# Kernel tuning notes

Measured on AMD Instinct MI355X. Metric: run time of the kernel, lower is better.

Reference implementation:

```python
import jax, jax.numpy as jnp
import numpy as np

C = 256       # in_channels
IC = 128      # inter_channels = C // 2
G = 4         # num_group
D = IC // G   # per-group channels = 32
B, H, W_ = 4, 56, 56
EPS = 1e-5


def conv1x1(x, w, b=None):
    # x: (B,Cin,H,W), w: (Cout,Cin)
    y = jnp.einsum('bchw,oc->bohw', x, w)
    if b is not None:
        y = y + b[None, :, None, None]
    return y


def bn(x, scale, bias, mean, var):
    inv = scale / jnp.sqrt(var + EPS)
    return x * inv[None, :, None, None] + (bias - mean * inv)[None, :, None, None]


def setup_inputs():
    key = jax.random.key(0)
    ks = jax.random.split(key, 16)
    r = lambda k, shape, s=0.05: jax.random.normal(k, shape, jnp.float32) * s
    C4 = C // 4
    return {
        'x': jax.random.normal(ks[0], (B, C, H, W_), jnp.float32),
        'g_w': r(ks[1], (IC, C)), 'g_b': r(ks[2], (IC,)),
        'theta_w': r(ks[3], (IC, C)), 'theta_b': r(ks[4], (IC,)),
        'phi_w': r(ks[5], (IC, C)), 'phi_b': r(ks[6], (IC,)),
        'W_w': r(ks[7], (C, IC)), 'W_b': r(ks[8], (C,)),
        'bnW_scale': jnp.ones((C,)), 'bnW_bias': jnp.zeros((C,)),
        'bnW_mean': jnp.zeros((C,)), 'bnW_var': jnp.ones((C,)),
        'ff1_w': r(ks[9], (C4, C)),
        'ffbn1_scale': jnp.ones((C4,)), 'ffbn1_bias': jnp.zeros((C4,)),
        'ffbn1_mean': jnp.zeros((C4,)), 'ffbn1_var': jnp.ones((C4,)),
        'ff2_w': r(ks[10], (C4, C4, 3, 3)),
        'ffbn2_scale': jnp.ones((C4,)), 'ffbn2_bias': jnp.zeros((C4,)),
        'ffbn2_mean': jnp.zeros((C4,)), 'ffbn2_var': jnp.ones((C4,)),
        'ff3_w': r(ks[11], (C, C4)),
        'ffbn3_scale': jnp.ones((C,)), 'ffbn3_bias': jnp.zeros((C,)),
        'ffbn3_mean': jnp.zeros((C,)), 'ffbn3_var': jnp.ones((C,)),
    }


def reference(x, g_w, g_b, theta_w, theta_b, phi_w, phi_b, W_w, W_b,
              bnW_scale, bnW_bias, bnW_mean, bnW_var,
              ff1_w, ffbn1_scale, ffbn1_bias, ffbn1_mean, ffbn1_var,
              ff2_w, ffbn2_scale, ffbn2_bias, ffbn2_mean, ffbn2_var,
              ff3_w, ffbn3_scale, ffbn3_bias, ffbn3_mean, ffbn3_var):
    b, c, h, w = x.shape
    n = h * w
    # grouped non-local attention: channels split into G groups of D
    gx = conv1x1(x, g_w, g_b).reshape(b, G, D, n)       # (B,G,D,N)
    tx = conv1x1(x, theta_w, theta_b).reshape(b, G, D, n)
    px = conv1x1(x, phi_w, phi_b).reshape(b, G, D, n)
    f = jnp.einsum('bgdn,bgdm->bgnm', tx, px)           # (B,G,N,N) scores
    attn = jax.nn.softmax(f, axis=-1)                   # softmax over keys (torch dim=2 on (b,N,N))
    yy = jnp.einsum('bgnm,bgdm->bgdn', attn, gx)        # (B,G,D,N)
    y_out = yy.reshape(b, IC, h, w)
    W_y = bn(conv1x1(y_out, W_w, W_b), bnW_scale, bnW_bias, bnW_mean, bnW_var)
    z = jax.nn.relu(W_y + x)
    # FPNFFConv bottleneck FFN (BN in eval mode)
    o = jax.nn.relu(bn(conv1x1(z, ff1_w), ffbn1_scale, ffbn1_bias, ffbn1_mean, ffbn1_var))
    o = jax.lax.conv_general_dilated(o, ff2_w, (1, 1), 'SAME',
                                     dimension_numbers=('NCHW', 'OIHW', 'NCHW'))
    o = jax.nn.relu(bn(o, ffbn2_scale, ffbn2_bias, ffbn2_mean, ffbn2_var))
    o = bn(conv1x1(o, ff3_w), ffbn3_scale, ffbn3_bias, ffbn3_mean, ffbn3_var)
    return jax.nn.relu(o + z)
```

## Files before the change

### kernel.cpp

```cpp
#include <hip/hip_runtime.h>
#include <hip/hip_bf16.h>

#define NPIX 3136
#define BB 4
#define LOG2E 1.4426950408889634f

typedef unsigned short u16;
typedef __bf16 bf16x8 __attribute__((ext_vector_type(8)));
typedef float f32x4 __attribute__((ext_vector_type(4)));

__device__ __forceinline__ float b2f(u16 u) {
  union { unsigned u; float f; } c; c.u = ((unsigned)u) << 16; return c.f;
}
__device__ __forceinline__ u16 f2b(float f) {
  __hip_bfloat16 h = __float2bfloat16(f);
  return *reinterpret_cast<u16*>(&h);
}
__device__ __forceinline__ unsigned pk2(float a, float b) {
  return (unsigned)f2b(a) | ((unsigned)f2b(b) << 16);
}
__device__ __forceinline__ f32x4 mfma(bf16x8 a, bf16x8 b, f32x4 c) {
  return __builtin_amdgcn_mfma_f32_16x16x32_bf16(a, b, c, 0, 0, 0);
}

template<int NSTEP, int NOT>
__device__ __forceinline__ void mf_gemm2(const u16* __restrict__ A0,
                                         const u16* __restrict__ A1,
                                         const u16* __restrict__ Brow, int sB,
                                         int lq, f32x4* acc) {
#pragma unroll
  for (int s = 0; s < NSTEP; ++s) {
    bf16x8 bf[NOT];
#pragma unroll
    for (int ot = 0; ot < NOT; ++ot)
      bf[ot] = *(const bf16x8*)(Brow + (size_t)ot * 16 * sB + s * 32 + lq * 8);
    bf16x8 a0 = *(const bf16x8*)(A0 + s * 32 + lq * 8);
    bf16x8 a1 = *(const bf16x8*)(A1 + s * 32 + lq * 8);
#pragma unroll
    for (int ot = 0; ot < NOT; ++ot) {
      acc[ot] = mfma(a0, bf[ot], acc[ot]);
      acc[NOT + ot] = mfma(a1, bf[ot], acc[NOT + ot]);
    }
  }
}

__global__ __launch_bounds__(256) void prep_kernel(
    const float* __restrict__ x, u16* __restrict__ xt,
    const float* __restrict__ gw, const float* __restrict__ tw,
    const float* __restrict__ pw, const float* __restrict__ Ww,
    const float* __restrict__ f1w, const float* __restrict__ f2w,
    const float* __restrict__ f3w,
    u16* __restrict__ gwb, u16* __restrict__ twb, u16* __restrict__ pwb,
    u16* __restrict__ Wwb, u16* __restrict__ f1b, u16* __restrict__ f3b,
    u16* __restrict__ f2p) {
  __shared__ u16 sT[64 * 65];
  const int id = blockIdx.x;
  if (id < 784) {
    const int b = id / 196, rest = id % 196;
    const int c0 = (rest / 49) * 64, n0 = (rest % 49) * 64;
    const int t = threadIdx.x;
#pragma unroll
    for (int cc = 0; cc < 4; ++cc) {
      int c = cc * 16 + (t >> 4), n4 = (t & 15) * 4;
      float4 v = *(const float4*)(x + ((size_t)(b * 256 + c0 + c)) * NPIX + n0 + n4);
      sT[c * 65 + n4 + 0] = f2b(v.x);
      sT[c * 65 + n4 + 1] = f2b(v.y);
      sT[c * 65 + n4 + 2] = f2b(v.z);
      sT[c * 65 + n4 + 3] = f2b(v.w);
    }
    __syncthreads();
#pragma unroll
    for (int nn = 0; nn < 4; ++nn) {
      int n = nn * 16 + (t >> 4), c4 = (t & 15) * 4;
      uint2 s;
      s.x = (unsigned)sT[(c4 + 0) * 65 + n] | ((unsigned)sT[(c4 + 1) * 65 + n] << 16);
      s.y = (unsigned)sT[(c4 + 2) * 65 + n] | ((unsigned)sT[(c4 + 3) * 65 + n] << 16);
      *(uint2*)(xt + ((size_t)b * NPIX + n0 + n) * 256 + c0 + c4) = s;
    }
  } else {
    for (int i = (id - 784) * 256 + threadIdx.x; i < 200704; i += 196 * 256) {
      int j = i;
      if (j < 32768) { gwb[j] = f2b(gw[j]); continue; } j -= 32768;
      if (j < 32768) { twb[j] = f2b(tw[j] * LOG2E); continue; } j -= 32768;
      if (j < 32768) { pwb[j] = f2b(pw[j]); continue; } j -= 32768;
      if (j < 32768) { Wwb[j] = f2b(Ww[j]); continue; } j -= 32768;
      if (j < 16384) { f1b[j] = f2b(f1w[j]); continue; } j -= 16384;
      if (j < 16384) { f3b[j] = f2b(f3w[j]); continue; } j -= 16384;
      int t = j >> 12, rem = j & 4095, co = rem >> 6, ci = rem & 63;
      f2p[j] = f2b(f2w[(co * 64 + ci) * 9 + t]);
    }
  }
}

__global__ __launch_bounds__(256) void proj_kernel(
    const u16* __restrict__ xt,
    const u16* __restrict__ gwb, const u16* __restrict__ twb, const u16* __restrict__ pwb,
    const float* __restrict__ gb, const float* __restrict__ tb, const float* __restrict__ pb,
    u16* __restrict__ gx, u16* __restrict__ Tq, u16* __restrict__ Pk) {
  const int b = blockIdx.z, oc = blockIdx.y, nb = blockIdx.x * 128;
  const int sec = oc >> 1, rbase = (oc & 1) * 64;
  const u16* wsel = sec == 0 ? gwb : (sec == 1 ? twb : pwb);
  const float* bsel = sec == 0 ? gb : (sec == 1 ? tb : pb);
  const int wv = threadIdx.x >> 6, lane = threadIdx.x & 63;
  const int lr = lane & 15, lq = lane >> 4;
  const int nrow0 = nb + wv * 32, nrow1 = nrow0 + 16;
  const int r0 = nrow0 + lr < NPIX ? nrow0 + lr : NPIX - 1;
  const int r1 = nrow1 + lr < NPIX ? nrow1 + lr : NPIX - 1;
  f32x4 acc[8] = {};
  mf_gemm2<8, 4>(xt + ((size_t)b * NPIX + r0) * 256,
                 xt + ((size_t)b * NPIX + r1) * 256,
                 wsel + (size_t)(rbase + lr) * 256, 256, lq, acc);
#pragma unroll
  for (int t = 0; t < 2; ++t) {
    const int qn = (t ? nrow1 : nrow0) + lq * 4;
    if (qn >= NPIX) continue;
#pragma unroll
    for (int ot = 0; ot < 4; ++ot) {
      const f32x4 a = acc[t * 4 + ot];
      const int o = rbase + ot * 16 + lr;
      float bias = bsel[o];
      if (sec == 1) bias *= LOG2E;
      if (sec == 0) {
        uint2 s;
        s.x = pk2(a[0] + bias, a[1] + bias);
        s.y = pk2(a[2] + bias, a[3] + bias);
        *(uint2*)(gx + ((size_t)b * 128 + o) * NPIX + qn) = s;
      } else {
        const int g = o >> 5, dl = o & 31;
        u16* dst = sec == 1 ? Tq : Pk;
        size_t base = (size_t)(b * 4 + g) * NPIX;
#pragma unroll
        for (int r = 0; r < 4; ++r)
          dst[(base + qn + r) * 32 + dl] = f2b(a[r] + bias);
      }
    }
  }
}

__global__ __launch_bounds__(256) void attn_kernel(
    const u16* __restrict__ Tq, const u16* __restrict__ Pk,
    const u16* __restrict__ gx, u16* __restrict__ OPb, float* __restrict__ LP) {
  __shared__ __align__(16) u16 Plds[4][32][40];
  const int bid = blockIdx.x;
  const int ks = bid / 400, rem = bid % 400;
  const int bg = rem / 25, qblk = rem % 25;
  const int b = bg >> 2, g = bg & 3;
  const int wave = threadIdx.x >> 6, lane = threadIdx.x & 63;
  const int lr = lane & 15, lq = lane >> 4;
  const int qbase = qblk * 128 + wave * 32;
  const int kc0 = ks * 448;
  const u16* Qp = Tq + (size_t)bg * NPIX * 32;
  const u16* Kp = Pk + (size_t)bg * NPIX * 32;
  const u16* Vp = gx + ((size_t)b * 128 + g * 32) * NPIX;

  bf16x8 qf[2];
#pragma unroll
  for (int qi = 0; qi < 2; ++qi) {
    int row = qbase + qi * 16 + lr;
    row = row < NPIX ? row : NPIX - 1;
    qf[qi] = *(const bf16x8*)(Qp + (size_t)row * 32 + lq * 8);
  }
  const f32x4 z4 = {0.f, 0.f, 0.f, 0.f};
  f32x4 O[2][2], Lf[2];
#pragma unroll
  for (int qi = 0; qi < 2; ++qi) { O[qi][0] = z4; O[qi][1] = z4; Lf[qi] = z4; }
  bf16x8 onef;
#pragma unroll
  for (int j = 0; j < 8; ++j) onef[j] = (__bf16)1.0f;

#pragma unroll 1
  for (int kc = kc0; kc < kc0 + 448; kc += 32) {
    bf16x8 kf0 = *(const bf16x8*)(Kp + (size_t)(kc + lr) * 32 + lq * 8);
    bf16x8 kf1 = *(const bf16x8*)(Kp + (size_t)(kc + 16 + lr) * 32 + lq * 8);
    f32x4 S[2][2];
    S[0][0] = mfma(qf[0], kf0, z4);
    S[0][1] = mfma(qf[0], kf1, z4);
    S[1][0] = mfma(qf[1], kf0, z4);
    S[1][1] = mfma(qf[1], kf1, z4);
#pragma unroll
    for (int qi = 0; qi < 2; ++qi)
#pragma unroll
      for (int kt = 0; kt < 2; ++kt)
#pragma unroll
        for (int r = 0; r < 4; ++r) {
          unsigned u = __builtin_bit_cast(unsigned, __builtin_exp2f(S[qi][kt][r]));
          Plds[wave][qi * 16 + lq * 4 + r][kt * 16 + lr] = (u16)(u >> 16);
        }
    bf16x8 pf0 = *(const bf16x8*)(&Plds[wave][lr][lq * 8]);
    bf16x8 pf1 = *(const bf16x8*)(&Plds[wave][16 + lr][lq * 8]);
    bf16x8 vf0 = *(const bf16x8*)(Vp + (size_t)lr * NPIX + kc + lq * 8);
    bf16x8 vf1 = *(const bf16x8*)(Vp + (size_t)(16 + lr) * NPIX + kc + lq * 8);
    O[0][0] = mfma(pf0, vf0, O[0][0]);
    O[0][1] = mfma(pf0, vf1, O[0][1]);
    O[1][0] = mfma(pf1, vf0, O[1][0]);
    O[1][1] = mfma(pf1, vf1, O[1][1]);
    Lf[0] = mfma(pf0, onef, Lf[0]);
    Lf[1] = mfma(pf1, onef, Lf[1]);
  }
  const size_t sbase = (size_t)(ks * 16 + bg) * NPIX;
#pragma unroll
  for (int qi = 0; qi < 2; ++qi) {
#pragma unroll
    for (int r = 0; r < 4; ++r) {
      int qrow = qbase + qi * 16 + lq * 4 + r;
      if (qrow < NPIX) {
        size_t ob = (sbase + qrow) * 32;
        OPb[ob + lr] = f2b(O[qi][0][r]);
        OPb[ob + 16 + lr] = f2b(O[qi][1][r]);
        if (lr == 0) LP[sbase + qrow] = Lf[qi][r];
      }
    }
  }
}

__global__ __launch_bounds__(512) void wz_kernel(
    const u16* __restrict__ OPb, const float* __restrict__ LP,
    const u16* __restrict__ Wwb, const float* __restrict__ Wb,
    const float* __restrict__ sc, const float* __restrict__ bi,
    const float* __restrict__ mu, const float* __restrict__ var,
    const float* __restrict__ x, u16* __restrict__ zt) {
  __shared__ float Ls[4][32];
  const int b = blockIdx.y, nb = blockIdx.x * 32;
  const int tid = threadIdx.x;
  if (tid < 128) {
    int g = tid >> 5, row = tid & 31;
    float l = 0.f;
#pragma unroll
    for (int ks = 0; ks < 7; ++ks)
      l += LP[(size_t)(ks * 16 + b * 4 + g) * NPIX + nb + row];
    Ls[g][row] = 1.0f / l;
  }
  __syncthreads();
  const int wave = tid >> 6, lane = tid & 63;
  const int lr = lane & 15, lq = lane >> 4;
  const int oc = wave & 3, tt = wave >> 2;
  const int nrow = nb + tt * 16;
  f32x4 acc[4][4] = {};
#pragma unroll
  for (int g = 0; g < 4; ++g) {
    bf16x8 bf[4];
#pragma unroll
    for (int ot = 0; ot < 4; ++ot)
      bf[ot] = *(const bf16x8*)(Wwb + (size_t)(oc * 64 + ot * 16 + lr) * 128 + g * 32 + lq * 8);
#pragma unroll
    for (int ks = 0; ks < 7; ++ks) {
      bf16x8 af = *(const bf16x8*)(OPb +
          ((size_t)(ks * 16 + b * 4 + g) * NPIX + nrow + lr) * 32 + lq * 8);
#pragma unroll
      for (int ot = 0; ot < 4; ++ot)
        acc[g][ot] = mfma(af, bf[ot], acc[g][ot]);
    }
  }
#pragma unroll
  for (int ot = 0; ot < 4; ++ot) {
    const int o = oc * 64 + ot * 16 + lr;
    float inv = sc[o] * rsqrtf(var[o] + 1e-5f);
    float off = bi[o] - mu[o] * inv + Wb[o] * inv;
    const int qn = nrow + lq * 4;
    float4 xr = *(const float4*)(x + ((size_t)b * 256 + o) * NPIX + qn);
    float xv[4] = {xr.x, xr.y, xr.z, xr.w};
#pragma unroll
    for (int r = 0; r < 4; ++r) {
      int row = tt * 16 + lq * 4 + r;
      float y = acc[0][ot][r] * Ls[0][row] + acc[1][ot][r] * Ls[1][row] +
                acc[2][ot][r] * Ls[2][row] + acc[3][ot][r] * Ls[3][row];
      float v = fmaxf(y * inv + off + xv[r], 0.f);
      zt[((size_t)b * NPIX + qn + r) * 256 + o] = f2b(v);
    }
  }
}

__global__ __launch_bounds__(256) void ff1_kernel(
    const u16* __restrict__ zt, const u16* __restrict__ f1b,
    const float* __restrict__ sc, const float* __restrict__ bi,
    const float* __restrict__ mu, const float* __restrict__ var,
    u16* __restrict__ o1t) {
  const int b = blockIdx.z, oc = blockIdx.y, nb = blockIdx.x * 128;
  const int wv = threadIdx.x >> 6, lane = threadIdx.x & 63;
  const int lr = lane & 15, lq = lane >> 4;
  const int nrow0 = nb + wv * 32, nrow1 = nrow0 + 16;
  const int r0 = nrow0 + lr < NPIX ? nrow0 + lr : NPIX - 1;
  const int r1 = nrow1 + lr < NPIX ? nrow1 + lr : NPIX - 1;
  f32x4 acc[4] = {};
  mf_gemm2<8, 2>(zt + ((size_t)b * NPIX + r0) * 256,
                 zt + ((size_t)b * NPIX + r1) * 256,
                 f1b + (size_t)(oc * 32 + lr) * 256, 256, lq, acc);
#pragma unroll
  for (int t = 0; t < 2; ++t) {
    const int qn = (t ? nrow1 : nrow0) + lq * 4;
    if (qn >= NPIX) continue;
#pragma unroll
    for (int ot = 0; ot < 2; ++ot) {
      const f32x4 a = acc[t * 2 + ot];
      const int o = oc * 32 + ot * 16 + lr;
      float inv = sc[o] * rsqrtf(var[o] + 1e-5f);
      float off = bi[o] - mu[o] * inv;
#pragma unroll
      for (int r = 0; r < 4; ++r) {
        float v = fmaxf(a[r] * inv + off, 0.f);
        o1t[((size_t)b * NPIX + qn + r) * 64 + o] = f2b(v);
      }
    }
  }
}

__global__ __launch_bounds__(256) void ff23_kernel(
    const u16* __restrict__ o1t, const u16* __restrict__ f2p,
    const float* __restrict__ s2, const float* __restrict__ bi2,
    const float* __restrict__ mu2, const float* __restrict__ var2,
    const u16* __restrict__ f3b,
    const float* __restrict__ s3, const float* __restrict__ bi3,
    const float* __restrict__ mu3, const float* __restrict__ var3,
    const u16* __restrict__ zt, float* __restrict__ out) {
  __shared__ __align__(16) u16 o2s[32][72];
  const int b = blockIdx.y, nb = blockIdx.x * 32;
  const int wv = threadIdx.x >> 6, lane = threadIdx.x & 63;
  const int lr = lane & 15, lq = lane >> 4;
  const int tt = wv >> 1, oh = wv & 1;
  const int n0 = nb + tt * 16 + lr;
  const int h0 = n0 / 56, w0 = n0 % 56;
  f32x4 acc2[2] = {};
#pragma unroll
  for (int t = 0; t < 9; ++t) {
    const int dh = t / 3 - 1, dw = t % 3 - 1;
    const bool valid = (h0 + dh) >= 0 && (h0 + dh) < 56 && (w0 + dw) >= 0 && (w0 + dw) < 56;
    const u16* A0 = o1t + ((size_t)b * NPIX + n0 + dh * 56 + dw) * 64;
    const u16* Br = f2p + (size_t)t * 4096 + (size_t)(oh * 32 + lr) * 64;
#pragma unroll
    for (int k2 = 0; k2 < 2; ++k2) {
      bf16x8 bf0 = *(const bf16x8*)(Br + k2 * 32 + lq * 8);
      bf16x8 bf1 = *(const bf16x8*)(Br + (size_t)16 * 64 + k2 * 32 + lq * 8);
      bf16x8 a0 = {};
      if (valid) a0 = *(const bf16x8*)(A0 + k2 * 32 + lq * 8);
      acc2[0] = mfma(a0, bf0, acc2[0]);
      acc2[1] = mfma(a0, bf1, acc2[1]);
    }
  }
#pragma unroll
  for (int ot = 0; ot < 2; ++ot) {
    const int o = oh * 32 + ot * 16 + lr;
    float inv = s2[o] * rsqrtf(var2[o] + 1e-5f);
    float off = bi2[o] - mu2[o] * inv;
#pragma unroll
    for (int r = 0; r < 4; ++r) {
      float v = fmaxf(acc2[ot][r] * inv + off, 0.f);
      o2s[tt * 16 + lq * 4 + r][o] = f2b(v);
    }
  }
  __syncthreads();
  const int obase = oh * 128;
  f32x4 acc3[8] = {};
#pragma unroll
  for (int s = 0; s < 2; ++s) {
    bf16x8 af = *(const bf16x8*)(&o2s[tt * 16 + lr][s * 32 + lq * 8]);
#pragma unroll
    for (int ot = 0; ot < 8; ++ot) {
      bf16x8 bf = *(const bf16x8*)(f3b + (size_t)(obase + ot * 16 + lr) * 64 + s * 32 + lq * 8);
      acc3[ot] = mfma(af, bf, acc3[ot]);
    }
  }
  const int qn = nb + tt * 16 + lq * 4;
#pragma unroll
  for (int ot = 0; ot < 8; ++ot) {
    const int o = obase + ot * 16 + lr;
    float inv = s3[o] * rsqrtf(var3[o] + 1e-5f);
    float off = bi3[o] - mu3[o] * inv;
    float4 s;
    float* sv = (float*)&s;
#pragma unroll
    for (int r = 0; r < 4; ++r) {
      float zres = b2f(zt[((size_t)b * NPIX + qn + r) * 256 + o]);
      sv[r] = fmaxf(acc3[ot][r] * inv + off + zres, 0.f);
    }
    *(float4*)(out + ((size_t)b * 256 + o) * NPIX + qn) = s;
  }
}

extern "C" void kernel_launch(void* const* d_in, const int* in_sizes, int n_in,
                              void* d_out, int out_size, void* d_ws, size_t ws_size,
                              hipStream_t stream) {
  const float* x    = (const float*)d_in[0];
  const float* gw   = (const float*)d_in[1];
  const float* gb   = (const float*)d_in[2];
  const float* tw   = (const float*)d_in[3];
  const float* tb   = (const float*)d_in[4];
  const float* pw   = (const float*)d_in[5];
  const float* pb   = (const float*)d_in[6];
  const float* Ww   = (const float*)d_in[7];
  const float* Wb   = (const float*)d_in[8];
  const float* bnWs = (const float*)d_in[9];
  const float* bnWb = (const float*)d_in[10];
  const float* bnWm = (const float*)d_in[11];
  const float* bnWv = (const float*)d_in[12];
  const float* f1w  = (const float*)d_in[13];
  const float* b1s  = (const float*)d_in[14];
  const float* b1b  = (const float*)d_in[15];
  const float* b1m  = (const float*)d_in[16];
  const float* b1v  = (const float*)d_in[17];
  const float* f2w  = (const float*)d_in[18];
  const float* b2s  = (const float*)d_in[19];
  const float* b2b  = (const float*)d_in[20];
  const float* b2m  = (const float*)d_in[21];
  const float* b2v  = (const float*)d_in[22];
  const float* f3w  = (const float*)d_in[23];
  const float* b3s  = (const float*)d_in[24];
  const float* b3b  = (const float*)d_in[25];
  const float* b3m  = (const float*)d_in[26];
  const float* b3v  = (const float*)d_in[27];
  float* out = (float*)d_out;

  u16* p = (u16*)d_ws;
  u16* xt  = p; p += (size_t)BB * NPIX * 256;
  u16* gwb = p; p += 128 * 256;
  u16* twb = p; p += 128 * 256;
  u16* pwb = p; p += 128 * 256;
  u16* Wwb = p; p += 256 * 128;
  u16* f1b = p; p += 64 * 256;
  u16* f3b = p; p += 256 * 64;
  u16* f2p = p; p += 9 * 64 * 64;
  u16* Tq  = p; p += (size_t)16 * NPIX * 32;
  u16* Pk  = p; p += (size_t)16 * NPIX * 32;
  u16* gx  = p; p += (size_t)BB * 128 * NPIX;
  u16* OPb = p; p += (size_t)7 * 16 * NPIX * 32;
  float* LP = (float*)p; p += (size_t)7 * 16 * NPIX * 2;
  u16* zt  = p; p += (size_t)BB * NPIX * 256;
  u16* o1t = p; p += (size_t)BB * NPIX * 64;

  prep_kernel<<<dim3(980), 256, 0, stream>>>(x, xt, gw, tw, pw, Ww, f1w, f2w, f3w,
                                             gwb, twb, pwb, Wwb, f1b, f3b, f2p);
  proj_kernel<<<dim3(25, 6, BB), 256, 0, stream>>>(xt, gwb, twb, pwb, gb, tb, pb,
                                                   gx, Tq, Pk);
  attn_kernel<<<dim3(2800), 256, 0, stream>>>(Tq, Pk, gx, OPb, LP);
  wz_kernel<<<dim3(98, BB), 512, 0, stream>>>(OPb, LP, Wwb, Wb,
                                              bnWs, bnWb, bnWm, bnWv, x, zt);
  ff1_kernel<<<dim3(25, 2, BB), 256, 0, stream>>>(zt, f1b, b1s, b1b, b1m, b1v, o1t);
  ff23_kernel<<<dim3(98, BB), 256, 0, stream>>>(o1t, f2p, b2s, b2b, b2m, b2v,
                                                f3b, b3s, b3b, b3m, b3v, zt, out);
}
```

Baseline: 250.0 us.

## Fuse ff1 conv into wz kernel and split attention launch in two

The ff1 1x1 conv, its BN and ReLU are folded into the W-projection kernel: the z tile is staged in shared memory and multiplied by the ff1 weights directly, so the separate ff1 kernel no longer re-reads z from global memory and one launch is removed. The attention kernel is also split into two launches over key-split ranges (4 and 3 splits) through a new offset argument. This lengthens the fused kernel and adds LDS use, and the extra attention launch adds launch overhead for no clear benefit.

New measurement: 255.5 us. 2.2% more time.

```diff
diff --git a/kernel.cpp b/kernel.cpp
--- a/kernel.cpp
+++ b/kernel.cpp
@@ -139,10 +139,11 @@
 
 __global__ __launch_bounds__(256) void attn_kernel(
     const u16* __restrict__ Tq, const u16* __restrict__ Pk,
-    const u16* __restrict__ gx, u16* __restrict__ OPb, float* __restrict__ LP) {
+    const u16* __restrict__ gx, u16* __restrict__ OPb, float* __restrict__ LP,
+    int ks0) {
   __shared__ __align__(16) u16 Plds[4][32][40];
   const int bid = blockIdx.x;
-  const int ks = bid / 400, rem = bid % 400;
+  const int ks = ks0 + bid / 400, rem = bid % 400;
   const int bg = rem / 25, qblk = rem % 25;
   const int b = bg >> 2, g = bg & 3;
   const int wave = threadIdx.x >> 6, lane = threadIdx.x & 63;
@@ -213,13 +214,18 @@
   }
 }
 
-__global__ __launch_bounds__(512) void wz_kernel(
+__global__ __launch_bounds__(512) void wz2_kernel(
     const u16* __restrict__ OPb, const float* __restrict__ LP,
     const u16* __restrict__ Wwb, const float* __restrict__ Wb,
     const float* __restrict__ sc, const float* __restrict__ bi,
     const float* __restrict__ mu, const float* __restrict__ var,
-    const float* __restrict__ x, u16* __restrict__ zt) {
+    const float* __restrict__ x,
+    const u16* __restrict__ f1b,
+    const float* __restrict__ s1, const float* __restrict__ bi1,
+    const float* __restrict__ mu1, const float* __restrict__ var1,
+    u16* __restrict__ zt, u16* __restrict__ o1t) {
   __shared__ float Ls[4][32];
+  __shared__ __align__(16) u16 zs[32 * 264];
   const int b = blockIdx.y, nb = blockIdx.x * 32;
   const int tid = threadIdx.x;
   if (tid < 128) {
@@ -265,42 +271,28 @@
       float y = acc[0][ot][r] * Ls[0][row] + acc[1][ot][r] * Ls[1][row] +
                 acc[2][ot][r] * Ls[2][row] + acc[3][ot][r] * Ls[3][row];
       float v = fmaxf(y * inv + off + xv[r], 0.f);
-      zt[((size_t)b * NPIX + qn + r) * 256 + o] = f2b(v);
-    }
-  }
-}
-
-__global__ __launch_bounds__(256) void ff1_kernel(
-    const u16* __restrict__ zt, const u16* __restrict__ f1b,
-    const float* __restrict__ sc, const float* __restrict__ bi,
-    const float* __restrict__ mu, const float* __restrict__ var,
-    u16* __restrict__ o1t) {
-  const int b = blockIdx.z, oc = blockIdx.y, nb = blockIdx.x * 128;
-  const int wv = threadIdx.x >> 6, lane = threadIdx.x & 63;
-  const int lr = lane & 15, lq = lane >> 4;
-  const int nrow0 = nb + wv * 32, nrow1 = nrow0 + 16;
-  const int r0 = nrow0 + lr < NPIX ? nrow0 + lr : NPIX - 1;
-  const int r1 = nrow1 + lr < NPIX ? nrow1 + lr : NPIX - 1;
-  f32x4 acc[4] = {};
-  mf_gemm2<8, 2>(zt + ((size_t)b * NPIX + r0) * 256,
-                 zt + ((size_t)b * NPIX + r1) * 256,
-                 f1b + (size_t)(oc * 32 + lr) * 256, 256, lq, acc);
-#pragma unroll
-  for (int t = 0; t < 2; ++t) {
-    const int qn = (t ? nrow1 : nrow0) + lq * 4;
-    if (qn >= NPIX) continue;
-#pragma unroll
-    for (int ot = 0; ot < 2; ++ot) {
-      const f32x4 a = acc[t * 2 + ot];
-      const int o = oc * 32 + ot * 16 + lr;
-      float inv = sc[o] * rsqrtf(var[o] + 1e-5f);
-      float off = bi[o] - mu[o] * inv;
-#pragma unroll
-      for (int r = 0; r < 4; ++r) {
-        float v = fmaxf(a[r] * inv + off, 0.f);
-        o1t[((size_t)b * NPIX + qn + r) * 64 + o] = f2b(v);
-      }
-    }
+      u16 vb = f2b(v);
+      zt[((size_t)b * NPIX + qn + r) * 256 + o] = vb;
+      zs[row * 264 + o] = vb;
+    }
+  }
+  __syncthreads();
+  const int tt2 = wave >> 2, oq = wave & 3;
+  f32x4 a1 = {0.f, 0.f, 0.f, 0.f};
+#pragma unroll
+  for (int s = 0; s < 8; ++s) {
+    bf16x8 af = *(const bf16x8*)(&zs[(tt2 * 16 + lr) * 264 + s * 32 + lq * 8]);
+    bf16x8 bf = *(const bf16x8*)(f1b + (size_t)(oq * 16 + lr) * 256 + s * 32 + lq * 8);
+    a1 = mfma(af, bf, a1);
+  }
+  const int o1 = oq * 16 + lr;
+  float inv1 = s1[o1] * rsqrtf(var1[o1] + 1e-5f);
+  float off1 = bi1[o1] - mu1[o1] * inv1;
+  const int qn2 = nb + tt2 * 16 + lq * 4;
+#pragma unroll
+  for (int r = 0; r < 4; ++r) {
+    float v = fmaxf(a1[r] * inv1 + off1, 0.f);
+    o1t[((size_t)b * NPIX + qn2 + r) * 64 + o1] = f2b(v);
   }
 }
 
@@ -430,10 +422,11 @@
                                              gwb, twb, pwb, Wwb, f1b, f3b, f2p);
   proj_kernel<<<dim3(25, 6, BB), 256, 0, stream>>>(xt, gwb, twb, pwb, gb, tb, pb,
                                                    gx, Tq, Pk);
-  attn_kernel<<<dim3(2800), 256, 0, stream>>>(Tq, Pk, gx, OPb, LP);
-  wz_kernel<<<dim3(98, BB), 512, 0, stream>>>(OPb, LP, Wwb, Wb,
-                                              bnWs, bnWb, bnWm, bnWv, x, zt);
-  ff1_kernel<<<dim3(25, 2, BB), 256, 0, stream>>>(zt, f1b, b1s, b1b, b1m, b1v, o1t);
+  attn_kernel<<<dim3(1600), 256, 0, stream>>>(Tq, Pk, gx, OPb, LP, 0);
+  attn_kernel<<<dim3(1200), 256, 0, stream>>>(Tq, Pk, gx, OPb, LP, 4);
+  wz2_kernel<<<dim3(98, BB), 512, 0, stream>>>(OPb, LP, Wwb, Wb,
+                                               bnWs, bnWb, bnWm, bnWv, x,
+                                               f1b, b1s, b1b, b1m, b1v, zt, o1t);
   ff23_kernel<<<dim3(98, BB), 256, 0, stream>>>(o1t, f2p, b2s, b2b, b2m, b2v,
                                                 f3b, b3s, b3b, b3m, b3v, zt, out);
 }
```
